# Optimization experiments

Hardware: AMD Instinct MI355X
Metric: run time of the kernel (lower is better)

## Reference

```python
import jax, jax.numpy as jnp
import numpy as np

WS = 8    # window size
DM = 64   # d_model
DI = 128  # d_inner = 2*d_model (expand=2)
DS = 16   # d_state
DR = 4    # dt_rank = ceil(d_model/16)
K = 4     # scan directions


def setup_inputs() -> dict:
    key = jax.random.key(0)
    ks = jax.random.split(key, 8)
    B, H, W = 2, 128, 128
    x = jax.random.normal(ks[0], (B, DM, H, W), jnp.float32)
    in_proj_w = jax.random.normal(ks[1], (2 * DI, DM), jnp.float32) * 0.02
    conv_w = jax.random.normal(ks[2], (DI, 1, 3, 3), jnp.float32) * 0.1
    conv_b = jnp.zeros((DI,), jnp.float32)
    x_proj_w = jax.random.normal(ks[3], (K, DR + 2 * DS, DI), jnp.float32) * 0.02
    dt_projs_w = jax.random.normal(ks[4], (K, DI, DR), jnp.float32) * 0.1
    dt_projs_b = jax.random.uniform(ks[5], (K, DI), jnp.float32, -6.0, -3.0)
    A_logs = jnp.log(jnp.tile(jnp.arange(1, DS + 1, dtype=jnp.float32), (K, DI, 1)))
    Ds = jnp.ones((K, DI), jnp.float32)
    ln_g = jnp.ones((DI,), jnp.float32)
    ln_b = jnp.zeros((DI,), jnp.float32)
    out_proj_w = jax.random.normal(ks[6], (DM, DI), jnp.float32) * 0.02
    return dict(x=x, in_proj_w=in_proj_w, conv_w=conv_w, conv_b=conv_b,
                x_proj_w=x_proj_w, dt_projs_w=dt_projs_w, dt_projs_b=dt_projs_b,
                A_logs=A_logs, Ds=Ds, ln_g=ln_g, ln_b=ln_b, out_proj_w=out_proj_w)


def _ss2d(x, in_proj_w, conv_w, conv_b, x_proj_w, dt_projs_w, dt_projs_b,
          A_logs, Ds, ln_g, ln_b, out_proj_w):
    # x: (Bw, DM, h, w) -- one 8x8 window per batch element
    Bw, _, h, w = x.shape
    L = h * w
    xhwc = x.transpose(0, 2, 3, 1)                      # (Bw,h,w,DM)
    xz = xhwc @ in_proj_w.T                             # (Bw,h,w,2*DI)
    xc, z = jnp.split(xz, 2, axis=-1)
    xc = xc.transpose(0, 3, 1, 2)                       # (Bw,DI,h,w)
    xc = jax.lax.conv_general_dilated(
        xc, conv_w, (1, 1), 'SAME', feature_group_count=DI,
        dimension_numbers=('NCHW', 'OIHW', 'NCHW')) + conv_b[None, :, None, None]
    xc = jax.nn.silu(xc)
    # 4-direction cross-scan: hw, wh, reversed hw, reversed wh
    x_hw = xc.reshape(Bw, DI, L)
    x_wh = xc.transpose(0, 1, 3, 2).reshape(Bw, DI, L)
    xs = jnp.stack([x_hw, x_wh, x_hw[..., ::-1], x_wh[..., ::-1]], axis=1)  # (Bw,K,DI,L)
    x_dbl = jnp.einsum('bkdl,kcd->bkcl', xs, x_proj_w)
    dt_lo, Bmat, Cmat = jnp.split(x_dbl, [DR, DR + DS], axis=2)
    dt = jnp.einsum('bkrl,kdr->bkdl', dt_lo, dt_projs_w)
    dt = jax.nn.softplus(dt + dt_projs_b[None, :, :, None])  # (Bw,K,DI,L)
    A = -jnp.exp(A_logs)                                     # (K,DI,DS)

    def step(hst, inp):
        u_t, dt_t, B_t, C_t = inp  # (Bw,K,DI),(Bw,K,DI),(Bw,K,DS),(Bw,K,DS)
        dA = jnp.exp(dt_t[..., None] * A)                       # (Bw,K,DI,DS)
        hst = hst * dA + (dt_t * u_t)[..., None] * B_t[:, :, None, :]
        y = jnp.einsum('bkds,bks->bkd', hst, C_t)
        return hst, y

    seq = (jnp.moveaxis(xs, -1, 0), jnp.moveaxis(dt, -1, 0),
           jnp.moveaxis(Bmat, -1, 0), jnp.moveaxis(Cmat, -1, 0))
    h0 = jnp.zeros((Bw, K, DI, DS), xs.dtype)
    _, ys = jax.lax.scan(step, h0, seq)                  # (L,Bw,K,DI)
    ys = jnp.moveaxis(ys, 0, -1) + Ds[None, :, :, None] * xs  # (Bw,K,DI,L)
    # merge directions (undo flips / wh transpose)
    y = (ys[:, 0]
         + ys[:, 2][..., ::-1]
         + ys[:, 1].reshape(Bw, DI, w, h).transpose(0, 1, 3, 2).reshape(Bw, DI, L)
         + ys[:, 3][..., ::-1].reshape(Bw, DI, w, h).transpose(0, 1, 3, 2).reshape(Bw, DI, L))
    y = y.reshape(Bw, DI, h, w).transpose(0, 2, 3, 1)    # (Bw,h,w,DI)
    mu = y.mean(-1, keepdims=True)
    var = y.var(-1, keepdims=True)
    y = (y - mu) * jax.lax.rsqrt(var + 1e-5) * ln_g + ln_b
    y = y * jax.nn.silu(z)
    out = y @ out_proj_w.T                               # (Bw,h,w,DM)
    return out.transpose(0, 3, 1, 2)


def reference(x, in_proj_w, conv_w, conv_b, x_proj_w, dt_projs_w, dt_projs_b,
              A_logs, Ds, ln_g, ln_b, out_proj_w):
    B, D, H, W = x.shape
    nh, nw = H // WS, W // WS
    # window partition: b d (nh hs) (nw ws) -> (b nh nw) d hs ws
    xw = x.reshape(B, D, nh, WS, nw, WS).transpose(0, 2, 4, 1, 3, 5)
    xw = xw.reshape(B * nh * nw, D, WS, WS)
    yw = _ss2d(xw, in_proj_w, conv_w, conv_b, x_proj_w, dt_projs_w, dt_projs_b,
               A_logs, Ds, ln_g, ln_b, out_proj_w)
    # window merge
    y = yw.reshape(B, nh, nw, D, WS, WS).transpose(0, 3, 1, 4, 2, 5)
    return y.reshape(B, D, H, W)
```

## Files before the change

kernel.cpp:

```cpp
#include <hip/hip_runtime.h>

#define L_HW (128*128)

__device__ __forceinline__ int transp(int p){ return ((p&7)<<3)|(p>>3); }

#define K1_XIN  0
#define K1_WBUF 4352
#define K1_XCP  8448
#define K1_XOUT 0
#define K1_SMEM 12608

__global__ __launch_bounds__(512, 4)
void k1_gemm(const float* __restrict__ x,
             const float* __restrict__ in_proj_w,
             const float* __restrict__ conv_w,
             const float* __restrict__ conv_b,
             float* __restrict__ xct_g,
             float* __restrict__ z_g)
{
    __shared__ float sm[K1_SMEM];
    const int t = threadIdx.x;
    const int win = blockIdx.x >> 2, q = blockIdx.x & 3;
    const int b = win >> 8, ih = (win >> 4) & 15, iw = win & 15;
    const float* xwin = x + ((size_t)b*64)*L_HW + ih*8*128 + iw*8;

    {
        const int ch = t >> 3, r = t & 7;
        const float* src = xwin + (size_t)ch*L_HW + r*128;
        float4 v0 = *(const float4*)(src);
        float4 v1 = *(const float4*)(src + 4);
        float* dst = sm + K1_XIN + ch;
        const int p0 = r*8;
        dst[(p0+0)*68]=v0.x; dst[(p0+1)*68]=v0.y; dst[(p0+2)*68]=v0.z; dst[(p0+3)*68]=v0.w;
        dst[(p0+4)*68]=v1.x; dst[(p0+5)*68]=v1.y; dst[(p0+6)*68]=v1.z; dst[(p0+7)*68]=v1.w;
    }
    {
        const float* wsrc = in_proj_w + q*4096;
        *(float4*)(sm + K1_WBUF + t*4)        = *(const float4*)(wsrc + t*4);
        *(float4*)(sm + K1_WBUF + (t+512)*4)  = *(const float4*)(wsrc + (t+512)*4);
    }
    __syncthreads();

    const int p = t & 63, og = t >> 6;
    float a0=0,a1=0,a2=0,a3=0,a4=0,a5=0,a6=0,a7=0;
    {
        const float* wrow = sm + K1_WBUF + og*8*64;
#define K1ACC(J, A) { float4 wv = *(const float4*)(wrow + (J)*64 + chq*4); \
        A = fmaf(xv.x,wv.x, fmaf(xv.y,wv.y, fmaf(xv.z,wv.z, fmaf(xv.w,wv.w, A)))); }
        #pragma unroll
        for (int chq = 0; chq < 16; ++chq) {
            float4 xv = *(const float4*)(sm + K1_XIN + p*68 + chq*4);
            K1ACC(0,a0) K1ACC(1,a1) K1ACC(2,a2) K1ACC(3,a3)
            K1ACC(4,a4) K1ACC(5,a5) K1ACC(6,a6) K1ACC(7,a7)
        }
#undef K1ACC
    }

    if (q >= 2) {
        float* zw = z_g + (size_t)win*8192 + ((q-2)*64)*64 + p;
        zw[(og*8+0)*64]=a0; zw[(og*8+1)*64]=a1; zw[(og*8+2)*64]=a2; zw[(og*8+3)*64]=a3;
        zw[(og*8+4)*64]=a4; zw[(og*8+5)*64]=a5; zw[(og*8+6)*64]=a6; zw[(og*8+7)*64]=a7;
        return;
    }

    {
        float* xp = sm + K1_XCP + og*8*65 + p;
        xp[0]=a0; xp[65]=a1; xp[130]=a2; xp[195]=a3;
        xp[260]=a4; xp[325]=a5; xp[390]=a6; xp[455]=a7;
    }
    __syncthreads();

    {
        const int dloc = t & 63, qq = t >> 6;
        const int dg = q*64 + dloc;
        const float* cwp = conv_w + dg*9;
        const float c0=cwp[0],c1=cwp[1],c2=cwp[2],c3=cwp[3],c4=cwp[4],
                    c5=cwp[5],c6=cwp[6],c7=cwp[7],c8=cwp[8];
        const float cb = conv_b[dg];
        const float* xc = sm + K1_XCP + dloc*65;
        #pragma unroll
        for (int jj = 0; jj < 8; ++jj) {
            const int px = qq*8 + jj;
            const int r = px >> 3, c = px & 7;
            float a = cb;
            if (r > 0) {
                if (c > 0) a = fmaf(xc[px-9], c0, a);
                a = fmaf(xc[px-8], c1, a);
                if (c < 7) a = fmaf(xc[px-7], c2, a);
            }
            if (c > 0) a = fmaf(xc[px-1], c3, a);
            a = fmaf(xc[px], c4, a);
            if (c < 7) a = fmaf(xc[px+1], c5, a);
            if (r < 7) {
                if (c > 0) a = fmaf(xc[px+7], c6, a);
                a = fmaf(xc[px+8], c7, a);
                if (c < 7) a = fmaf(xc[px+9], c8, a);
            }
            sm[K1_XOUT + px*68 + dloc] = a / (1.f + __expf(-a));
        }
    }
    __syncthreads();

    {
        float* dst = xct_g + (size_t)win*8192 + q*64;
        #pragma unroll
        for (int i = 0; i < 2; ++i) {
            const int idx4 = i*512 + t;
            const int pp = idx4 >> 4, dg = idx4 & 15;
            float4 v = *(const float4*)(sm + K1_XOUT + pp*68 + dg*4);
            *(float4*)(dst + pp*128 + dg*4) = v;
        }
    }
}

#define K2_WL 4096
#define K2_XD 6400
#define K2_SMEM 8768

__global__ __launch_bounds__(256, 4)
void k2_xproj(const float* __restrict__ xct_g,
              const float* __restrict__ x_proj_w,
              float* __restrict__ xdbl_g)
{
    __shared__ float sm[K2_SMEM];
    const int t = threadIdx.x;
    const int win = blockIdx.x >> 2, k = blockIdx.x & 3;
    const int p = t & 63, jg = t >> 6;
    float a0=0,a1=0,a2=0,a3=0,a4=0,a5=0,a6=0,a7=0,a8=0;

    for (int h = 0; h < 2; ++h) {
        __syncthreads();
        #pragma unroll
        for (int i = 0; i < 4; ++i) {
            const int idx4 = i*256 + t;
            const int pp = idx4 >> 4, dg = idx4 & 15;
            float4 v = *(const float4*)(xct_g + (size_t)win*8192 + pp*128 + h*64 + dg*4);
            *(float4*)(sm + pp*64 + ((dg ^ (pp&7))<<2)) = v;
        }
        #pragma unroll
        for (int i = 0; i < 3; ++i) {
            const int idx4 = i*256 + t;
            if (idx4 < 576) {
                const int r = idx4 >> 4, dg = idx4 & 15;
                float4 v = *(const float4*)(x_proj_w + (size_t)(k*36 + r)*128 + h*64 + dg*4);
                *(float4*)(sm + K2_WL + r*64 + dg*4) = v;
            }
        }
        __syncthreads();
        const float* wb = sm + K2_WL + jg*9*64;
#define K2ACC(J, A) { float4 wv = *(const float4*)(wb + (J)*64 + dg*4); \
        A = fmaf(xv.x,wv.x, fmaf(xv.y,wv.y, fmaf(xv.z,wv.z, fmaf(xv.w,wv.w, A)))); }
        #pragma unroll
        for (int dg = 0; dg < 16; ++dg) {
            float4 xv = *(const float4*)(sm + p*64 + ((dg ^ (p&7))<<2));
            K2ACC(0,a0) K2ACC(1,a1) K2ACC(2,a2) K2ACC(3,a3) K2ACC(4,a4)
            K2ACC(5,a5) K2ACC(6,a6) K2ACC(7,a7) K2ACC(8,a8)
        }
#undef K2ACC
    }
    __syncthreads();

    {
        const int l = (k==0) ? p : (k==1) ? transp(p) : (k==2) ? (63-p) : (63 - transp(p));
        float* dp = sm + K2_XD + l*37 + jg*9;
        dp[0]=a0; dp[1]=a1; dp[2]=a2; dp[3]=a3; dp[4]=a4;
        dp[5]=a5; dp[6]=a6; dp[7]=a7; dp[8]=a8;
    }
    __syncthreads();

    {
        float* dst = xdbl_g + ((size_t)win*4 + k)*2304;
        #pragma unroll
        for (int i = 0; i < 9; ++i) {
            const int idx = i*256 + t;
            const int l2 = idx / 36, c = idx - l2*36;
            dst[idx] = sm[K2_XD + l2*37 + c];
        }
    }
}

#define F_XD 0
#define F_YC 9216
#define F_YM 11264
#define F_MU 19584
#define F_RS 19648
#define F_SMEM 19712

#define HSTEP(I, E, BC, CC, Y) { h##I = fmaf(h##I, (E), dtu*(BC)); Y = fmaf(h##I, (CC), Y); }

__global__ __launch_bounds__(512, 4)
void k3_all(const float* __restrict__ xct_g,
            const float* __restrict__ z_g,
            const float* __restrict__ xdbl_g,
            const float* __restrict__ dt_projs_w,
            const float* __restrict__ dt_projs_b,
            const float* __restrict__ A_logs,
            const float* __restrict__ Ds,
            const float* __restrict__ ln_g,
            const float* __restrict__ ln_b,
            const float* __restrict__ out_proj_w,
            float* __restrict__ out)
{
    __shared__ float sm[F_SMEM];
    const int t = threadIdx.x;
    const int win = blockIdx.x;

    #pragma unroll
    for (int i = 0; i < 5; ++i) {
        const int idx4 = i*512 + t;
        if (idx4 < 2304) {
            float4 v = *(const float4*)(xdbl_g + (size_t)win*9216 + idx4*4);
            *(float4*)(sm + F_XD + idx4*4) = v;
        }
    }
    for (int i = t; i < 8320; i += 512) sm[F_YM + i] = 0.f;

    const int k = t >> 7, d = t & 127;
    const int kd = t;
    const float* alp = A_logs + kd*16;
    const float A0 = -__expf(alp[0]);
    bool fastp = true;
    #pragma unroll
    for (int s = 1; s < 16; ++s) {
        float a = -__expf(alp[s]);
        fastp = fastp && (fabsf(a - (float)(s+1)*A0) <= 1e-4f * fabsf(a));
    }
    const int allfast = __syncthreads_and(fastp ? 1 : 0);

    const float4 wv = *(const float4*)(dt_projs_w + kd*4);
    const float dtb = dt_projs_b[kd];
    float h0=0,h1=0,h2=0,h3=0,h4=0,h5=0,h6=0,h7=0,
          h8=0,h9=0,h10=0,h11=0,h12=0,h13=0,h14=0,h15=0;
    const float* XDk = sm + F_XD + k*2304;
    const float* ub = xct_g + (size_t)win*8192 + d;

#define MERGE_CHUNK(C) { \
        __syncthreads(); \
        if (t < 128) { \
            const int dd = t; \
            float* ymr = sm + F_YM + dd*65; \
            _Pragma("unroll") \
            for (int j = 0; j < 4; ++j) { \
                const int l = (C)*4 + j; \
                const int lr = 63 - l; \
                const float* ycb = sm + F_YC + j*512 + dd; \
                ymr[l]          += ycb[0]; \
                ymr[transp(l)]  += ycb[128]; \
                ymr[lr]         += ycb[256]; \
                ymr[transp(lr)] += ycb[384]; \
            } \
        } \
        __syncthreads(); }

    if (allfast) {
        for (int c = 0; c < 16; ++c) {
            #pragma unroll
            for (int j = 0; j < 4; ++j) {
                const int l = c*4 + j;
                const float* row = XDk + l*36;
                float4 d4 = *(const float4*)(row);
                float4 b0 = *(const float4*)(row+4),  float4_b1 = *(const float4*)(row+8);
                float4 b2 = *(const float4*)(row+12), b3 = *(const float4*)(row+16);
                float4 c0 = *(const float4*)(row+20), c1 = *(const float4*)(row+24);
                float4 c2 = *(const float4*)(row+28), c3 = *(const float4*)(row+32);
                float dtraw = dtb + wv.x*d4.x + wv.y*d4.y + wv.z*d4.z + wv.w*d4.w;
                float dt = (dtraw > 20.f) ? dtraw : __logf(1.f + __expf(dtraw));
                const int lr = 63 - l;
                const int p = (k==0)?l : (k==1)?transp(l) : (k==2)?lr : transp(lr);
                const float u = ub[p*128];
                const float dtu = dt * u;
                const float r  = __expf(dt * A0);
                const float r2 = r*r, r4 = r2*r2, r8 = r4*r4;
                const float e3 = r2*r, e5 = r4*r, e6 = r4*r2, e7 = r4*e3;
                const float e9 = r8*r, e10 = r8*r2, e11 = r8*e3, e12 = r8*r4;
                const float e13 = r8*e5, e14 = r8*e6, e15 = r8*e7, e16 = r8*r8;
                float ay0 = 0.f, ay1 = 0.f, ay2 = 0.f, ay3 = 0.f;
                HSTEP(0,  r,   b0.x, c0.x, ay0)  HSTEP(1,  r2,  b0.y, c0.y, ay1)
                HSTEP(2,  e3,  b0.z, c0.z, ay2)  HSTEP(3,  r4,  b0.w, c0.w, ay3)
                HSTEP(4,  e5,  float4_b1.x, c1.x, ay0)  HSTEP(5,  e6,  float4_b1.y, c1.y, ay1)
                HSTEP(6,  e7,  float4_b1.z, c1.z, ay2)  HSTEP(7,  r8,  float4_b1.w, c1.w, ay3)
                HSTEP(8,  e9,  b2.x, c2.x, ay0)  HSTEP(9,  e10, b2.y, c2.y, ay1)
                HSTEP(10, e11, b2.z, c2.z, ay2)  HSTEP(11, e12, b2.w, c2.w, ay3)
                HSTEP(12, e13, b3.x, c3.x, ay0)  HSTEP(13, e14, b3.y, c3.y, ay1)
                HSTEP(14, e15, b3.z, c3.z, ay2)  HSTEP(15, e16, b3.w, c3.w, ay3)
                sm[F_YC + j*512 + t] = (ay0 + ay1) + (ay2 + ay3);
            }
            MERGE_CHUNK(c)
        }
    } else {
        const float A1=-__expf(alp[1]), A2=-__expf(alp[2]), A3=-__expf(alp[3]),
                    A4=-__expf(alp[4]), A5=-__expf(alp[5]), A6=-__expf(alp[6]),
                    A7=-__expf(alp[7]), A8=-__expf(alp[8]), A9=-__expf(alp[9]),
                    A10=-__expf(alp[10]), A11=-__expf(alp[11]), A12=-__expf(alp[12]),
                    A13=-__expf(alp[13]), A14=-__expf(alp[14]), A15=-__expf(alp[15]);
        for (int c = 0; c < 16; ++c) {
            #pragma unroll
            for (int j = 0; j < 4; ++j) {
                const int l = c*4 + j;
                const float* row = XDk + l*36;
                float4 d4 = *(const float4*)(row);
                float4 b0 = *(const float4*)(row+4),  float4_b1 = *(const float4*)(row+8);
                float4 b2 = *(const float4*)(row+12), b3 = *(const float4*)(row+16);
                float4 c0 = *(const float4*)(row+20), c1 = *(const float4*)(row+24);
                float4 c2 = *(const float4*)(row+28), c3 = *(const float4*)(row+32);
                float dtraw = dtb + wv.x*d4.x + wv.y*d4.y + wv.z*d4.z + wv.w*d4.w;
                float dt = (dtraw > 20.f) ? dtraw : __logf(1.f + __expf(dtraw));
                const int lr = 63 - l;
                const int p = (k==0)?l : (k==1)?transp(l) : (k==2)?lr : transp(lr);
                const float u = ub[p*128];
                const float dtu = dt * u;
                float ay0 = 0.f, ay1 = 0.f, ay2 = 0.f, ay3 = 0.f;
                HSTEP(0,  __expf(dt*A0),  b0.x, c0.x, ay0)  HSTEP(1,  __expf(dt*A1),  b0.y, c0.y, ay1)
                HSTEP(2,  __expf(dt*A2),  b0.z, c0.z, ay2)  HSTEP(3,  __expf(dt*A3),  b0.w, c0.w, ay3)
                HSTEP(4,  __expf(dt*A4),  float4_b1.x, c1.x, ay0)  HSTEP(5,  __expf(dt*A5),  float4_b1.y, c1.y, ay1)
                HSTEP(6,  __expf(dt*A6),  float4_b1.z, c1.z, ay2)  HSTEP(7,  __expf(dt*A7),  float4_b1.w, c1.w, ay3)
                HSTEP(8,  __expf(dt*A8),  b2.x, c2.x, ay0)  HSTEP(9,  __expf(dt*A9),  b2.y, c2.y, ay1)
                HSTEP(10, __expf(dt*A10), b2.z, c2.z, ay2)  HSTEP(11, __expf(dt*A11), b2.w, c2.w, ay3)
                HSTEP(12, __expf(dt*A12), b3.x, c3.x, ay0)  HSTEP(13, __expf(dt*A13), b3.y, c3.y, ay1)
                HSTEP(14, __expf(dt*A14), b3.z, c3.z, ay2)  HSTEP(15, __expf(dt*A15), b3.w, c3.w, ay3)
                sm[F_YC + j*512 + t] = (ay0 + ay1) + (ay2 + ay3);
            }
            MERGE_CHUNK(c)
        }
    }
#undef MERGE_CHUNK

    {
        const int d2 = t & 127, pq = t >> 7;
        const float Dsum = Ds[d2] + Ds[128+d2] + Ds[256+d2] + Ds[384+d2];
        const float* uc = xct_g + (size_t)win*8192 + d2;
        #pragma unroll
        for (int i = 0; i < 16; ++i) {
            const int p = pq*16 + i;
            sm[F_YM + d2*65 + p] += Dsum * uc[p*128];
        }
    }
    __syncthreads();

    {
        const int px = t >> 3, j = t & 7;
        float s1 = 0.f, s2 = 0.f;
        #pragma unroll
        for (int i = 0; i < 16; ++i) {
            float v = sm[F_YM + (j*16 + i)*65 + px];
            s1 += v; s2 += v*v;
        }
        s1 += __shfl_xor(s1,1); s2 += __shfl_xor(s2,1);
        s1 += __shfl_xor(s1,2); s2 += __shfl_xor(s2,2);
        s1 += __shfl_xor(s1,4); s2 += __shfl_xor(s2,4);
        if (j == 0) {
            float mu  = s1 * 0.0078125f;
            float var = s2 * 0.0078125f - mu*mu;
            sm[F_MU + px] = mu;
            sm[F_RS + px] = rsqrtf(var + 1e-5f);
        }
    }
    __syncthreads();

    {
        const int p = t & 63, dblk = (t >> 6) * 16;
        const float mu = sm[F_MU + p], rs = sm[F_RS + p];
        const float* zb = z_g + (size_t)win*8192 + p;
        #pragma unroll
        for (int i = 0; i < 16; ++i) {
            const int dd = dblk + i;
            float yv = sm[F_YM + dd*65 + p];
            float yh = (yv - mu)*rs*ln_g[dd] + ln_b[dd];
            float zv = zb[dd*64];
            sm[F_YM + dd*65 + p] = yh * (zv / (1.f + __expf(-zv)));
        }
    }
    __syncthreads();

    {
        const int p = t & 63, m0 = (t >> 6) * 8;
        float o0=0,o1=0,o2=0,o3=0,o4=0,o5=0,o6=0,o7=0;
#define OACC(J, O) { float4 wq = *(const float4*)(out_proj_w + (m0+(J))*128 + dq*4); \
        O = fmaf(y0,wq.x, fmaf(y1,wq.y, fmaf(y2,wq.z, fmaf(y3,wq.w, O)))); }
        #pragma unroll
        for (int dq = 0; dq < 32; ++dq) {
            float y0 = sm[F_YM + (dq*4+0)*65 + p];
            float y1 = sm[F_YM + (dq*4+1)*65 + p];
            float y2 = sm[F_YM + (dq*4+2)*65 + p];
            float y3 = sm[F_YM + (dq*4+3)*65 + p];
            OACC(0,o0) OACC(1,o1) OACC(2,o2) OACC(3,o3)
            OACC(4,o4) OACC(5,o5) OACC(6,o6) OACC(7,o7)
        }
#undef OACC
        const int b = win >> 8, ih = (win>>4)&15, iw = win&15;
        float* op = out + ((size_t)b*64)*L_HW + (ih*8 + (p>>3))*128 + iw*8 + (p&7);
        op[(size_t)(m0+0)*L_HW]=o0; op[(size_t)(m0+1)*L_HW]=o1;
        op[(size_t)(m0+2)*L_HW]=o2; op[(size_t)(m0+3)*L_HW]=o3;
        op[(size_t)(m0+4)*L_HW]=o4; op[(size_t)(m0+5)*L_HW]=o5;
        op[(size_t)(m0+6)*L_HW]=o6; op[(size_t)(m0+7)*L_HW]=o7;
    }
}
#undef HSTEP

extern "C" void kernel_launch(void* const* d_in, const int* in_sizes, int n_in,
                              void* d_out, int out_size, void* d_ws, size_t ws_size,
                              hipStream_t stream) {
    const float* x          = (const float*)d_in[0];
    const float* in_proj_w  = (const float*)d_in[1];
    const float* conv_w     = (const float*)d_in[2];
    const float* conv_b     = (const float*)d_in[3];
    const float* x_proj_w   = (const float*)d_in[4];
    const float* dt_projs_w = (const float*)d_in[5];
    const float* dt_projs_b = (const float*)d_in[6];
    const float* A_logs     = (const float*)d_in[7];
    const float* Ds         = (const float*)d_in[8];
    const float* ln_g       = (const float*)d_in[9];
    const float* ln_b       = (const float*)d_in[10];
    const float* out_proj_w = (const float*)d_in[11];
    float* out = (float*)d_out;

    float* xct  = (float*)d_ws;
    float* zb   = xct + 4194304;
    float* xdbl = zb  + 4194304;

    k1_gemm<<<dim3(2048), dim3(512), 0, stream>>>(x, in_proj_w, conv_w, conv_b, xct, zb);
    k2_xproj<<<dim3(2048), dim3(256), 0, stream>>>(xct, x_proj_w, xdbl);
    k3_all<<<dim3(512), dim3(512), 0, stream>>>(
        xct, zb, xdbl, dt_projs_w, dt_projs_b, A_logs, Ds, ln_g, ln_b,
        out_proj_w, out);
}
```

Baseline: 164.1 us.

## Split fused scan kernel into per-direction scan and separate post-processing kernel

```diff
diff --git a/kernel.cpp b/kernel.cpp
--- a/kernel.cpp
+++ b/kernel.cpp
@@ -179,44 +179,31 @@
     }
 }
 
-#define F_XD 0
-#define F_YC 9216
-#define F_YM 11264
-#define F_MU 19584
-#define F_RS 19648
-#define F_SMEM 19712
-
 #define HSTEP(I, E, BC, CC, Y) { h##I = fmaf(h##I, (E), dtu*(BC)); Y = fmaf(h##I, (CC), Y); }
 
-__global__ __launch_bounds__(512, 4)
-void k3_all(const float* __restrict__ xct_g,
-            const float* __restrict__ z_g,
-            const float* __restrict__ xdbl_g,
-            const float* __restrict__ dt_projs_w,
-            const float* __restrict__ dt_projs_b,
-            const float* __restrict__ A_logs,
-            const float* __restrict__ Ds,
-            const float* __restrict__ ln_g,
-            const float* __restrict__ ln_b,
-            const float* __restrict__ out_proj_w,
-            float* __restrict__ out)
+__global__ __launch_bounds__(128, 4)
+void k3a_scan(const float* __restrict__ xct_g,
+              const float* __restrict__ xdbl_g,
+              const float* __restrict__ dt_projs_w,
+              const float* __restrict__ dt_projs_b,
+              const float* __restrict__ A_logs,
+              float* __restrict__ y_g)
 {
-    __shared__ float sm[F_SMEM];
+    __shared__ float sm[2304];
     const int t = threadIdx.x;
-    const int win = blockIdx.x;
+    const int win = blockIdx.x >> 2, k = blockIdx.x & 3;
 
     #pragma unroll
     for (int i = 0; i < 5; ++i) {
-        const int idx4 = i*512 + t;
-        if (idx4 < 2304) {
-            float4 v = *(const float4*)(xdbl_g + (size_t)win*9216 + idx4*4);
-            *(float4*)(sm + F_XD + idx4*4) = v;
-        }
-    }
-    for (int i = t; i < 8320; i += 512) sm[F_YM + i] = 0.f;
-
-    const int k = t >> 7, d = t & 127;
-    const int kd = t;
+        const int idx4 = i*128 + t;
+        if (idx4 < 576) {
+            float4 v = *(const float4*)(xdbl_g + ((size_t)win*4 + k)*2304 + idx4*4);
+            *(float4*)(sm + idx4*4) = v;
+        }
+    }
+
+    const int d = t;
+    const int kd = k*128 + d;
     const float* alp = A_logs + kd*16;
     const float A0 = -__expf(alp[0]);
     bool fastp = true;
@@ -231,61 +218,38 @@
     const float dtb = dt_projs_b[kd];
     float h0=0,h1=0,h2=0,h3=0,h4=0,h5=0,h6=0,h7=0,
           h8=0,h9=0,h10=0,h11=0,h12=0,h13=0,h14=0,h15=0;
-    const float* XDk = sm + F_XD + k*2304;
     const float* ub = xct_g + (size_t)win*8192 + d;
-
-#define MERGE_CHUNK(C) { \
-        __syncthreads(); \
-        if (t < 128) { \
-            const int dd = t; \
-            float* ymr = sm + F_YM + dd*65; \
-            _Pragma("unroll") \
-            for (int j = 0; j < 4; ++j) { \
-                const int l = (C)*4 + j; \
-                const int lr = 63 - l; \
-                const float* ycb = sm + F_YC + j*512 + dd; \
-                ymr[l]          += ycb[0]; \
-                ymr[transp(l)]  += ycb[128]; \
-                ymr[lr]         += ycb[256]; \
-                ymr[transp(lr)] += ycb[384]; \
-            } \
-        } \
-        __syncthreads(); }
+    float* yw = y_g + ((size_t)win*4 + k)*8192 + d;
 
     if (allfast) {
-        for (int c = 0; c < 16; ++c) {
-            #pragma unroll
-            for (int j = 0; j < 4; ++j) {
-                const int l = c*4 + j;
-                const float* row = XDk + l*36;
-                float4 d4 = *(const float4*)(row);
-                float4 b0 = *(const float4*)(row+4),  float4_b1 = *(const float4*)(row+8);
-                float4 b2 = *(const float4*)(row+12), b3 = *(const float4*)(row+16);
-                float4 c0 = *(const float4*)(row+20), c1 = *(const float4*)(row+24);
-                float4 c2 = *(const float4*)(row+28), c3 = *(const float4*)(row+32);
-                float dtraw = dtb + wv.x*d4.x + wv.y*d4.y + wv.z*d4.z + wv.w*d4.w;
-                float dt = (dtraw > 20.f) ? dtraw : __logf(1.f + __expf(dtraw));
-                const int lr = 63 - l;
-                const int p = (k==0)?l : (k==1)?transp(l) : (k==2)?lr : transp(lr);
-                const float u = ub[p*128];
-                const float dtu = dt * u;
-                const float r  = __expf(dt * A0);
-                const float r2 = r*r, r4 = r2*r2, r8 = r4*r4;
-                const float e3 = r2*r, e5 = r4*r, e6 = r4*r2, e7 = r4*e3;
-                const float e9 = r8*r, e10 = r8*r2, e11 = r8*e3, e12 = r8*r4;
-                const float e13 = r8*e5, e14 = r8*e6, e15 = r8*e7, e16 = r8*r8;
-                float ay0 = 0.f, ay1 = 0.f, ay2 = 0.f, ay3 = 0.f;
-                HSTEP(0,  r,   b0.x, c0.x, ay0)  HSTEP(1,  r2,  b0.y, c0.y, ay1)
-                HSTEP(2,  e3,  b0.z, c0.z, ay2)  HSTEP(3,  r4,  b0.w, c0.w, ay3)
-                HSTEP(4,  e5,  float4_b1.x, c1.x, ay0)  HSTEP(5,  e6,  float4_b1.y, c1.y, ay1)
-                HSTEP(6,  e7,  float4_b1.z, c1.z, ay2)  HSTEP(7,  r8,  float4_b1.w, c1.w, ay3)
-                HSTEP(8,  e9,  b2.x, c2.x, ay0)  HSTEP(9,  e10, b2.y, c2.y, ay1)
-                HSTEP(10, e11, b2.z, c2.z, ay2)  HSTEP(11, e12, b2.w, c2.w, ay3)
-                HSTEP(12, e13, b3.x, c3.x, ay0)  HSTEP(13, e14, b3.y, c3.y, ay1)
-                HSTEP(14, e15, b3.z, c3.z, ay2)  HSTEP(15, e16, b3.w, c3.w, ay3)
-                sm[F_YC + j*512 + t] = (ay0 + ay1) + (ay2 + ay3);
-            }
-            MERGE_CHUNK(c)
+        for (int l = 0; l < 64; ++l) {
+            const float* row = sm + l*36;
+            float4 d4 = *(const float4*)(row);
+            float4 b0 = *(const float4*)(row+4),  b1 = *(const float4*)(row+8);
+            float4 b2 = *(const float4*)(row+12), b3 = *(const float4*)(row+16);
+            float4 c0 = *(const float4*)(row+20), c1 = *(const float4*)(row+24);
+            float4 c2 = *(const float4*)(row+28), c3 = *(const float4*)(row+32);
+            float dtraw = dtb + wv.x*d4.x + wv.y*d4.y + wv.z*d4.z + wv.w*d4.w;
+            float dt = (dtraw > 20.f) ? dtraw : __logf(1.f + __expf(dtraw));
+            const int lr = 63 - l;
+            const int p = (k==0)?l : (k==1)?transp(l) : (k==2)?lr : transp(lr);
+            const float u = ub[p*128];
+            const float dtu = dt * u;
+            const float r  = __expf(dt * A0);
+            const float r2 = r*r, r4 = r2*r2, r8 = r4*r4;
+            const float e3 = r2*r, e5 = r4*r, e6 = r4*r2, e7 = r4*e3;
+            const float e9 = r8*r, e10 = r8*r2, e11 = r8*e3, e12 = r8*r4;
+            const float e13 = r8*e5, e14 = r8*e6, e15 = r8*e7, e16 = r8*r8;
+            float ay0=0.f, ay1=0.f, ay2=0.f, ay3=0.f;
+            HSTEP(0,  r,   b0.x, c0.x, ay0)  HSTEP(1,  r2,  b0.y, c0.y, ay1)
+            HSTEP(2,  e3,  b0.z, c0.z, ay2)  HSTEP(3,  r4,  b0.w, c0.w, ay3)
+            HSTEP(4,  e5,  b1.x, c1.x, ay0)  HSTEP(5,  e6,  b1.y, c1.y, ay1)
+            HSTEP(6,  e7,  b1.z, c1.z, ay2)  HSTEP(7,  r8,  b1.w, c1.w, ay3)
+            HSTEP(8,  e9,  b2.x, c2.x, ay0)  HSTEP(9,  e10, b2.y, c2.y, ay1)
+            HSTEP(10, e11, b2.z, c2.z, ay2)  HSTEP(11, e12, b2.w, c2.w, ay3)
+            HSTEP(12, e13, b3.x, c3.x, ay0)  HSTEP(13, e14, b3.y, c3.y, ay1)
+            HSTEP(14, e15, b3.z, c3.z, ay2)  HSTEP(15, e16, b3.w, c3.w, ay3)
+            yw[l*128] = (ay0 + ay1) + (ay2 + ay3);
         }
     } else {
         const float A1=-__expf(alp[1]), A2=-__expf(alp[2]), A3=-__expf(alp[3]),
@@ -293,109 +257,143 @@
                     A7=-__expf(alp[7]), A8=-__expf(alp[8]), A9=-__expf(alp[9]),
                     A10=-__expf(alp[10]), A11=-__expf(alp[11]), A12=-__expf(alp[12]),
                     A13=-__expf(alp[13]), A14=-__expf(alp[14]), A15=-__expf(alp[15]);
-        for (int c = 0; c < 16; ++c) {
-            #pragma unroll
-            for (int j = 0; j < 4; ++j) {
-                const int l = c*4 + j;
-                const float* row = XDk + l*36;
-                float4 d4 = *(const float4*)(row);
-                float4 b0 = *(const float4*)(row+4),  float4_b1 = *(const float4*)(row+8);
-                float4 b2 = *(const float4*)(row+12), b3 = *(const float4*)(row+16);
-                float4 c0 = *(const float4*)(row+20), c1 = *(const float4*)(row+24);
-                float4 c2 = *(const float4*)(row+28), c3 = *(const float4*)(row+32);
-                float dtraw = dtb + wv.x*d4.x + wv.y*d4.y + wv.z*d4.z + wv.w*d4.w;
-                float dt = (dtraw > 20.f) ? dtraw : __logf(1.f + __expf(dtraw));
-                const int lr = 63 - l;
-                const int p = (k==0)?l : (k==1)?transp(l) : (k==2)?lr : transp(lr);
-                const float u = ub[p*128];
-                const float dtu = dt * u;
-                float ay0 = 0.f, ay1 = 0.f, ay2 = 0.f, ay3 = 0.f;
-                HSTEP(0,  __expf(dt*A0),  b0.x, c0.x, ay0)  HSTEP(1,  __expf(dt*A1),  b0.y, c0.y, ay1)
-                HSTEP(2,  __expf(dt*A2),  b0.z, c0.z, ay2)  HSTEP(3,  __expf(dt*A3),  b0.w, c0.w, ay3)
-                HSTEP(4,  __expf(dt*A4),  float4_b1.x, c1.x, ay0)  HSTEP(5,  __expf(dt*A5),  float4_b1.y, c1.y, ay1)
-                HSTEP(6,  __expf(dt*A6),  float4_b1.z, c1.z, ay2)  HSTEP(7,  __expf(dt*A7),  float4_b1.w, c1.w, ay3)
-                HSTEP(8,  __expf(dt*A8),  b2.x, c2.x, ay0)  HSTEP(9,  __expf(dt*A9),  b2.y, c2.y, ay1)
-                HSTEP(10, __expf(dt*A10), b2.z, c2.z, ay2)  HSTEP(11, __expf(dt*A11), b2.w, c2.w, ay3)
-                HSTEP(12, __expf(dt*A12), b3.x, c3.x, ay0)  HSTEP(13, __expf(dt*A13), b3.y, c3.y, ay1)
-                HSTEP(14, __expf(dt*A14), b3.z, c3.z, ay2)  HSTEP(15, __expf(dt*A15), b3.w, c3.w, ay3)
-                sm[F_YC + j*512 + t] = (ay0 + ay1) + (ay2 + ay3);
-            }
-            MERGE_CHUNK(c)
-        }
-    }
-#undef MERGE_CHUNK
-
-    {
-        const int d2 = t & 127, pq = t >> 7;
-        const float Dsum = Ds[d2] + Ds[128+d2] + Ds[256+d2] + Ds[384+d2];
-        const float* uc = xct_g + (size_t)win*8192 + d2;
-        #pragma unroll
-        for (int i = 0; i < 16; ++i) {
-            const int p = pq*16 + i;
-            sm[F_YM + d2*65 + p] += Dsum * uc[p*128];
-        }
-    }
-    __syncthreads();
-
-    {
-        const int px = t >> 3, j = t & 7;
+        for (int l = 0; l < 64; ++l) {
+            const float* row = sm + l*36;
+            float4 d4 = *(const float4*)(row);
+            float4 b0 = *(const float4*)(row+4),  b1 = *(const float4*)(row+8);
+            float4 b2 = *(const float4*)(row+12), b3 = *(const float4*)(row+16);
+            float4 c0 = *(const float4*)(row+20), c1 = *(const float4*)(row+24);
+            float4 c2 = *(const float4*)(row+28), c3 = *(const float4*)(row+32);
+            float dtraw = dtb + wv.x*d4.x + wv.y*d4.y + wv.z*d4.z + wv.w*d4.w;
+            float dt = (dtraw > 20.f) ? dtraw : __logf(1.f + __expf(dtraw));
+            const int lr = 63 - l;
+            const int p = (k==0)?l : (k==1)?transp(l) : (k==2)?lr : transp(lr);
+            const float u = ub[p*128];
+            const float dtu = dt * u;
+            float ay0=0.f, ay1=0.f, ay2=0.f, ay3=0.f;
+            HSTEP(0,  __expf(dt*A0),  b0.x, c0.x, ay0)  HSTEP(1,  __expf(dt*A1),  b0.y, c0.y, ay1)
+            HSTEP(2,  __expf(dt*A2),  b0.z, c0.z, ay2)  HSTEP(3,  __expf(dt*A3),  b0.w, c0.w, ay3)
+            HSTEP(4,  __expf(dt*A4),  b1.x, c1.x, ay0)  HSTEP(5,  __expf(dt*A5),  b1.y, c1.y, ay1)
+            HSTEP(6,  __expf(dt*A6),  b1.z, c1.z, ay2)  HSTEP(7,  __expf(dt*A7),  b1.w, c1.w, ay3)
+            HSTEP(8,  __expf(dt*A8),  b2.x, c2.x, ay0)  HSTEP(9,  __expf(dt*A9),  b2.y, c2.y, ay1)
+            HSTEP(10, __expf(dt*A10), b2.z, c2.z, ay2)  HSTEP(11, __expf(dt*A11), b2.w, c2.w, ay3)
+            HSTEP(12, __expf(dt*A12), b3.x, c3.x, ay0)  HSTEP(13, __expf(dt*A13), b3.y, c3.y, ay1)
+            HSTEP(14, __expf(dt*A14), b3.z, c3.z, ay2)  HSTEP(15, __expf(dt*A15), b3.w, c3.w, ay3)
+            yw[l*128] = (ay0 + ay1) + (ay2 + ay3);
+        }
+    }
+}
+#undef HSTEP
+
+#define B_YM 0
+#define B_MU 2112
+#define B_RS 2128
+#define B_SMEM 2144
+
+__global__ __launch_bounds__(256, 8)
+void k3b_post(const float* __restrict__ y_g,
+              const float* __restrict__ xct_g,
+              const float* __restrict__ z_g,
+              const float* __restrict__ Ds,
+              const float* __restrict__ ln_g,
+              const float* __restrict__ ln_b,
+              const float* __restrict__ out_proj_w,
+              float* __restrict__ out)
+{
+    __shared__ float sm[B_SMEM];
+    const int t = threadIdx.x;
+    const int win = blockIdx.x >> 2, pq = blockIdx.x & 3;
+
+    {
+        const int px = t & 15, dc = t >> 4;
+        const int P = pq*16 + px;
+        const int tp = transp(P);
+        const int d0 = dc*8;
+        const float* yb = y_g + (size_t)win*4*8192;
+        const float* r0 = yb + (size_t)0*8192 + P*128 + d0;
+        const float* r1 = yb + (size_t)1*8192 + tp*128 + d0;
+        const float* r2 = yb + (size_t)2*8192 + (63-P)*128 + d0;
+        const float* r3 = yb + (size_t)3*8192 + (63-tp)*128 + d0;
+        const float* uu = xct_g + (size_t)win*8192 + P*128 + d0;
+        float* ymr = sm + B_YM + px*132 + d0;
+        #pragma unroll
+        for (int h = 0; h < 2; ++h) {
+            float4 a = *(const float4*)(r0 + h*4);
+            float4 bb = *(const float4*)(r1 + h*4);
+            float4 cc = *(const float4*)(r2 + h*4);
+            float4 ee = *(const float4*)(r3 + h*4);
+            float4 uv = *(const float4*)(uu + h*4);
+            const int dd = d0 + h*4;
+            float4 rv;
+            rv.x = a.x+bb.x+cc.x+ee.x + (Ds[dd+0]+Ds[128+dd+0]+Ds[256+dd+0]+Ds[384+dd+0])*uv.x;
+            rv.y = a.y+bb.y+cc.y+ee.y + (Ds[dd+1]+Ds[128+dd+1]+Ds[256+dd+1]+Ds[384+dd+1])*uv.y;
+            rv.z = a.z+bb.z+cc.z+ee.z + (Ds[dd+2]+Ds[128+dd+2]+Ds[256+dd+2]+Ds[384+dd+2])*uv.z;
+            rv.w = a.w+bb.w+cc.w+ee.w + (Ds[dd+3]+Ds[128+dd+3]+Ds[256+dd+3]+Ds[384+dd+3])*uv.w;
+            *(float4*)(ymr + h*4) = rv;
+        }
+    }
+    __syncthreads();
+
+    {
+        const int px = t >> 4, j = t & 15;
         float s1 = 0.f, s2 = 0.f;
         #pragma unroll
-        for (int i = 0; i < 16; ++i) {
-            float v = sm[F_YM + (j*16 + i)*65 + px];
+        for (int i = 0; i < 8; ++i) {
+            float v = sm[B_YM + px*132 + j*8 + i];
             s1 += v; s2 += v*v;
         }
         s1 += __shfl_xor(s1,1); s2 += __shfl_xor(s2,1);
         s1 += __shfl_xor(s1,2); s2 += __shfl_xor(s2,2);
         s1 += __shfl_xor(s1,4); s2 += __shfl_xor(s2,4);
+        s1 += __shfl_xor(s1,8); s2 += __shfl_xor(s2,8);
         if (j == 0) {
             float mu  = s1 * 0.0078125f;
             float var = s2 * 0.0078125f - mu*mu;
-            sm[F_MU + px] = mu;
-            sm[F_RS + px] = rsqrtf(var + 1e-5f);
-        }
-    }
-    __syncthreads();
-
-    {
-        const int p = t & 63, dblk = (t >> 6) * 16;
-        const float mu = sm[F_MU + p], rs = sm[F_RS + p];
-        const float* zb = z_g + (size_t)win*8192 + p;
-        #pragma unroll
-        for (int i = 0; i < 16; ++i) {
-            const int dd = dblk + i;
-            float yv = sm[F_YM + dd*65 + p];
+            sm[B_MU + px] = mu;
+            sm[B_RS + px] = rsqrtf(var + 1e-5f);
+        }
+    }
+    __syncthreads();
+
+    {
+        const int px = t & 15, dc = t >> 4;
+        const int P = pq*16 + px;
+        const float mu = sm[B_MU + px], rs = sm[B_RS + px];
+        const float* zb = z_g + (size_t)win*8192 + P;
+        #pragma unroll
+        for (int i = 0; i < 8; ++i) {
+            const int dd = dc*8 + i;
+            float yv = sm[B_YM + px*132 + dd];
             float yh = (yv - mu)*rs*ln_g[dd] + ln_b[dd];
             float zv = zb[dd*64];
-            sm[F_YM + dd*65 + p] = yh * (zv / (1.f + __expf(-zv)));
-        }
-    }
-    __syncthreads();
-
-    {
-        const int p = t & 63, m0 = (t >> 6) * 8;
-        float o0=0,o1=0,o2=0,o3=0,o4=0,o5=0,o6=0,o7=0;
-#define OACC(J, O) { float4 wq = *(const float4*)(out_proj_w + (m0+(J))*128 + dq*4); \
-        O = fmaf(y0,wq.x, fmaf(y1,wq.y, fmaf(y2,wq.z, fmaf(y3,wq.w, O)))); }
+            sm[B_YM + px*132 + dd] = yh * (zv / (1.f + __expf(-zv)));
+        }
+    }
+    __syncthreads();
+
+    {
+        const int px = t & 15, mg = t >> 4;
+        const int P = pq*16 + px;
+        const float* ymr = sm + B_YM + px*132;
+        float o0=0,o1=0,o2=0,o3=0;
         #pragma unroll
         for (int dq = 0; dq < 32; ++dq) {
-            float y0 = sm[F_YM + (dq*4+0)*65 + p];
-            float y1 = sm[F_YM + (dq*4+1)*65 + p];
-            float y2 = sm[F_YM + (dq*4+2)*65 + p];
-            float y3 = sm[F_YM + (dq*4+3)*65 + p];
-            OACC(0,o0) OACC(1,o1) OACC(2,o2) OACC(3,o3)
-            OACC(4,o4) OACC(5,o5) OACC(6,o6) OACC(7,o7)
-        }
-#undef OACC
+            float4 y4 = *(const float4*)(ymr + dq*4);
+            float4 w0 = *(const float4*)(out_proj_w + (mg*4+0)*128 + dq*4);
+            float4 w1 = *(const float4*)(out_proj_w + (mg*4+1)*128 + dq*4);
+            float4 w2 = *(const float4*)(out_proj_w + (mg*4+2)*128 + dq*4);
+            float4 w3 = *(const float4*)(out_proj_w + (mg*4+3)*128 + dq*4);
+            o0 = fmaf(y4.x,w0.x, fmaf(y4.y,w0.y, fmaf(y4.z,w0.z, fmaf(y4.w,w0.w, o0))));
+            o1 = fmaf(y4.x,w1.x, fmaf(y4.y,w1.y, fmaf(y4.z,w1.z, fmaf(y4.w,w1.w, o1))));
+            o2 = fmaf(y4.x,w2.x, fmaf(y4.y,w2.y, fmaf(y4.z,w2.z, fmaf(y4.w,w2.w, o2))));
+            o3 = fmaf(y4.x,w3.x, fmaf(y4.y,w3.y, fmaf(y4.z,w3.z, fmaf(y4.w,w3.w, o3))));
+        }
         const int b = win >> 8, ih = (win>>4)&15, iw = win&15;
-        float* op = out + ((size_t)b*64)*L_HW + (ih*8 + (p>>3))*128 + iw*8 + (p&7);
-        op[(size_t)(m0+0)*L_HW]=o0; op[(size_t)(m0+1)*L_HW]=o1;
-        op[(size_t)(m0+2)*L_HW]=o2; op[(size_t)(m0+3)*L_HW]=o3;
-        op[(size_t)(m0+4)*L_HW]=o4; op[(size_t)(m0+5)*L_HW]=o5;
-        op[(size_t)(m0+6)*L_HW]=o6; op[(size_t)(m0+7)*L_HW]=o7;
+        float* op = out + ((size_t)b*64)*L_HW + (ih*8 + (P>>3))*128 + iw*8 + (P&7);
+        op[(size_t)(mg*4+0)*L_HW]=o0; op[(size_t)(mg*4+1)*L_HW]=o1;
+        op[(size_t)(mg*4+2)*L_HW]=o2; op[(size_t)(mg*4+3)*L_HW]=o3;
     }
 }
-#undef HSTEP
 
 extern "C" void kernel_launch(void* const* d_in, const int* in_sizes, int n_in,
                               void* d_out, int out_size, void* d_ws, size_t ws_size,
@@ -417,10 +415,12 @@
     float* xct  = (float*)d_ws;
     float* zb   = xct + 4194304;
     float* xdbl = zb  + 4194304;
+    float* yg   = xdbl + 1179648;
 
     k1_gemm<<<dim3(2048), dim3(512), 0, stream>>>(x, in_proj_w, conv_w, conv_b, xct, zb);
     k2_xproj<<<dim3(2048), dim3(256), 0, stream>>>(xct, x_proj_w, xdbl);
-    k3_all<<<dim3(512), dim3(512), 0, stream>>>(
-        xct, zb, xdbl, dt_projs_w, dt_projs_b, A_logs, Ds, ln_g, ln_b,
-        out_proj_w, out);
+    k3a_scan<<<dim3(2048), dim3(128), 0, stream>>>(
+        xct, xdbl, dt_projs_w, dt_projs_b, A_logs, yg);
+    k3b_post<<<dim3(2048), dim3(256), 0, stream>>>(
+        yg, xct, zb, Ds, ln_g, ln_b, out_proj_w, out);
 }
```

Measured after the change: 204.6 us. +24.7%, slower.
